# Kernel tuning notes

Hardware: AMD Instinct MI355X
Metric: run time of the kernel (lower is better)

## Reference

```python
import jax, jax.numpy as jnp
import numpy as np

N, E, D, H = 50000, 800000, 128, 8
HD = D // H
EPS = 1e-5


def _layernorm(x, w, b):
    # Custom LayerNorm from the repo: divides by (unbiased std + eps), not sqrt(var+eps)
    mu = x.mean(axis=-1, keepdims=True)
    sd = x.std(axis=-1, keepdims=True, ddof=1)
    return (x - mu) / (sd + EPS) * w + b


def setup_inputs() -> dict:
    key = jax.random.key(0)
    ks = jax.random.split(key, 16)
    s = 1.0 / np.sqrt(D)
    inp = {
        "feats": jax.random.normal(ks[0], (N, D), jnp.float32),
        "edge_index": jax.random.randint(ks[1], (E, 2), 0, N, jnp.int32),
        "Wq": jax.random.normal(ks[2], (D, D), jnp.float32) * s,
        "bq": jnp.zeros((D,), jnp.float32),
        "Wk": jax.random.normal(ks[3], (D, D), jnp.float32) * s,
        "bk": jnp.zeros((D,), jnp.float32),
        "Wv": jax.random.normal(ks[4], (D, D), jnp.float32) * s,
        "bv": jnp.zeros((D,), jnp.float32),
        "Wo": jax.random.normal(ks[5], (D, D), jnp.float32) * s,
        "bo": jnp.zeros((D,), jnp.float32),
        "ln1_w": jnp.ones((D,), jnp.float32),
        "ln1_b": jnp.zeros((D,), jnp.float32),
        "ln2_w": jnp.ones((D,), jnp.float32),
        "ln2_b": jnp.zeros((D,), jnp.float32),
        "W1": jax.random.normal(ks[6], (4 * D, D), jnp.float32) * s,
        "b1": jnp.zeros((4 * D,), jnp.float32),
        "W2": jax.random.normal(ks[7], (D, 4 * D), jnp.float32) * (1.0 / np.sqrt(4 * D)),
        "b2": jnp.zeros((D,), jnp.float32),
    }
    return inp


def reference(feats, edge_index, Wq, bq, Wk, bk, Wv, bv, Wo, bo,
              ln1_w, ln1_b, ln2_w, ln2_b, W1, b1, W2, b2):
    n = feats.shape[0]
    row, col = edge_index[:, 0], edge_index[:, 1]

    # --- multi-head dot-product attention over edges (dropout = identity, eval mode) ---
    x2 = _layernorm(feats, ln1_w, ln1_b)
    q = (x2 @ Wq.T + bq).reshape(n, H, HD)
    k = (x2 @ Wk.T + bk).reshape(n, H, HD)
    v = (x2 @ Wv.T + bv).reshape(n, H, HD)

    # per-edge scores: q[col] . k[row] / sqrt(head_dim)  -> [E, H]
    scores = jnp.einsum('ehd,ehd->eh', q[col], k[row]) / np.sqrt(HD).astype(np.float32)

    # scatter softmax normalized over groups of `row`
    smax = jax.ops.segment_max(scores, row, num_segments=n)       # [N, H]
    ex = jnp.exp(scores - smax[row])                              # [E, H]
    denom = jax.ops.segment_sum(ex, row, num_segments=n)         # [N, H]
    alpha = ex / denom[row]                                       # [E, H]

    # weighted messages, aggregated at col via scatter_add
    msg = alpha[:, :, None] * v[row]                              # [E, H, HD]
    agg = jax.ops.segment_sum(msg, col, num_segments=n).reshape(n, D)
    att = agg @ Wo.T + bo

    feats = feats + att  # residual 1

    # --- MLP block: note ReLU after BOTH linears (fc_dims=[4D, D], D != 1) ---
    x2 = _layernorm(feats, ln2_w, ln2_b)
    h = jax.nn.relu(x2 @ W1.T + b1)
    h = jax.nn.relu(h @ W2.T + b2)
    feats = feats + h  # residual 2
    return feats
```

## Files before the change

kernel.cpp:

```cpp
#include <hip/hip_runtime.h>
#include <hip/hip_bf16.h>
#include <math.h>

#define H_HEADS 8
constexpr float LN_EPS = 1e-5f;
constexpr int NBCH = 64;
constexpr int NSEG = 4;

using short8 = __attribute__((ext_vector_type(8))) short;
using f32x4  = __attribute__((ext_vector_type(4))) float;
using half2v = __attribute__((ext_vector_type(2))) _Float16;

#if defined(__has_builtin)
#  if __has_builtin(__builtin_amdgcn_fdot2)
#    define HAS_FDOT2 1
#  endif
#endif
#ifndef HAS_FDOT2
#  define HAS_FDOT2 0
#endif

__device__ __forceinline__ ushort f2bf(float v){
  __hip_bfloat16 h = __float2bfloat16(v);
  return *reinterpret_cast<ushort*>(&h);
}
__device__ __forceinline__ float bf2f(ushort u){
  return __uint_as_float(((unsigned)u) << 16);
}

__device__ __forceinline__ void stage16(const ushort* g, ushort* l){
  __builtin_amdgcn_global_load_lds((const __attribute__((address_space(1))) unsigned*)g,
                                   (__attribute__((address_space(3))) unsigned*)l,
                                   16, 0, 0);
}

__global__ void ln_kernel(const float* __restrict__ x, const float* __restrict__ w,
                          const float* __restrict__ b, ushort* __restrict__ out, int nrows){
  int wid = threadIdx.x >> 6, lane = threadIdx.x & 63;
  int r = blockIdx.x * (blockDim.x >> 6) + wid;
  if (r >= nrows) return;
  float2 v = ((const float2*)(x + (size_t)r*128))[lane];
  float s = v.x + v.y;
  #pragma unroll
  for (int o = 32; o; o >>= 1) s += __shfl_xor(s, o);
  float mu = s * (1.0f/128.0f);
  float d0 = v.x - mu, d1 = v.y - mu;
  float ss = d0*d0 + d1*d1;
  #pragma unroll
  for (int o = 32; o; o >>= 1) ss += __shfl_xor(ss, o);
  float sd = sqrtf(ss * (1.0f/127.0f));
  float inv = 1.0f / (sd + LN_EPS);
  float2 wv = ((const float2*)w)[lane];
  float2 bv = ((const float2*)b)[lane];
  ushort2 o2 = { f2bf(d0*inv*wv.x + bv.x), f2bf(d1*inv*wv.y + bv.y) };
  ((ushort2*)(out + (size_t)r*128))[lane] = o2;
}

struct CvtArgs { const float* s[6]; ushort* d[6]; int cnt[6]; };
__global__ void cvt6_kernel(CvtArgs a){
  int w = blockIdx.y;
  int i = blockIdx.x*blockDim.x + threadIdx.x;
  if (i < a.cnt[w]) a.d[w][i] = f2bf(a.s[w][i]);
}

template<int K, int RELU, int RESID, int OUTMODE>
__device__ __forceinline__ void gemm_lds_body(
    const ushort* __restrict__ A, const ushort* __restrict__ W,
    const float* __restrict__ bias, const float* __restrict__ resid,
    void* __restrict__ out, int M, int Nout, int cb, ushort* Wl){
  constexpr int NCH = K / 128;
  int t = threadIdx.x;
  int wid = t >> 6, lane = t & 63;
  int mb = blockIdx.x * 128 + wid * 16;
  int lrow = lane & 15, kgrp = lane >> 4;
  int row = mb + lrow;
  bool waveok = mb < M;
  bool rowok = row < M;
  const ushort* arow = A + (size_t)(rowok ? row : (M-1)) * K + kgrp*8;

  f32x4 acc[8] = {};
  short8 af[2][4];

  #pragma unroll
  for (int p = 0; p < 4; ++p){
    int L = p*512 + t;
    int colp = L >> 4, sp = L & 15;
    stage16(W + (size_t)colp*K + ((sp ^ (colp & 7)) << 3),
            (ushort*)((char*)Wl + ((size_t)(p*512 + (t & ~63)))*16));
  }
  if (waveok){
    #pragma unroll
    for (int kk = 0; kk < 4; ++kk)
      af[0][kk] = *(const short8*)(arow + kk*32);
  }

  #pragma unroll
  for (int ci = 0; ci < NCH; ++ci){
    __syncthreads();
    int cur = ci & 1;
    if (waveok){
      if (ci + 1 < NCH){
        #pragma unroll
        for (int kk = 0; kk < 4; ++kk)
          af[cur^1][kk] = *(const short8*)(arow + (ci+1)*128 + kk*32);
      }
      #pragma unroll
      for (int kk = 0; kk < 4; ++kk){
        #pragma unroll
        for (int nt = 0; nt < 8; ++nt){
          int colc = nt*16 + lrow;
          int g = kk*4 + kgrp;
          short8 bfv = *(const short8*)((const char*)Wl + colc*256 + ((g ^ (colc & 7))*16));
          acc[nt] = __builtin_amdgcn_mfma_f32_16x16x32_bf16(af[cur][kk], bfv, acc[nt], 0, 0, 0);
        }
      }
    }
    if (ci + 1 < NCH){
      __syncthreads();
      const ushort* Wc = W + (ci+1)*128;
      #pragma unroll
      for (int p = 0; p < 4; ++p){
        int L = p*512 + t;
        int colp = L >> 4, sp = L & 15;
        stage16(Wc + (size_t)colp*K + ((sp ^ (colp & 7)) << 3),
                (ushort*)((char*)Wl + ((size_t)(p*512 + (t & ~63)))*16));
      }
    }
  }
  if (!waveok) return;

  int r0 = mb + kgrp*4;
  #pragma unroll
  for (int nt = 0; nt < 8; ++nt){
    int c = cb + nt*16 + lrow;
    float bsum = bias[c];
    #pragma unroll
    for (int i = 0; i < 4; ++i){
      int r = r0 + i;
      if (r >= M) continue;
      float v = acc[nt][i] + bsum;
      if (RELU)  v = fmaxf(v, 0.0f);
      if (RESID) v += resid[(size_t)r*Nout + c];
      if (OUTMODE == 1) ((ushort*)out)[(size_t)r*Nout + c] = f2bf(v);
      else if (OUTMODE == 2){
        _Float16 hv = (_Float16)v;
        ((ushort*)out)[(size_t)r*Nout + c] = __builtin_bit_cast(ushort, hv);
      } else ((float*)out)[(size_t)r*Nout + c] = v;
    }
  }
}

template<int K, int RELU, int RESID, int OUTMODE>
__global__ __launch_bounds__(512) void gemm_lds(
    const ushort* __restrict__ A, const ushort* __restrict__ Wfull,
    const float* __restrict__ bias, const float* __restrict__ resid,
    void* __restrict__ out, int M, int Nout){
  __shared__ __align__(16) ushort Wl[16384];
  int cb = blockIdx.y * 128;
  gemm_lds_body<K,RELU,RESID,OUTMODE>(A, Wfull + (size_t)cb*K, bias, resid, out, M, Nout, cb, Wl);
}

__global__ __launch_bounds__(512) void qkv_lds(
    const ushort* __restrict__ A, const ushort* __restrict__ Wcat,
    const float* __restrict__ bq, const float* __restrict__ bk, const float* __restrict__ bv,
    ushort* __restrict__ qb, ushort* __restrict__ kb, ushort* __restrict__ vb, int M){
  __shared__ __align__(16) ushort Wl[16384];
  int y = blockIdx.y;
  const float* bias = (y==0) ? bq : (y==1) ? bk : bv;
  ushort* out = (y==0) ? qb : (y==1) ? kb : vb;
  if (y == 2)
    gemm_lds_body<128,0,0,1>(A, Wcat + (size_t)y*16384, bias, nullptr, out, M, 128, 0, Wl);
  else
    gemm_lds_body<128,0,0,2>(A, Wcat + (size_t)y*16384, bias, nullptr, out, M, 128, 0, Wl);
}

__global__ __launch_bounds__(512) void gemm_wo_ln2(
    const ushort* __restrict__ A, const ushort* __restrict__ W,
    const float* __restrict__ bias, const float* __restrict__ feats,
    const float* __restrict__ lnw, const float* __restrict__ lnb,
    float* __restrict__ outp, ushort* __restrict__ x2b, int M){
  constexpr int K = 128;
  __shared__ __align__(16) ushort Wl[16384];
  int t = threadIdx.x;
  int wid = t >> 6, lane = t & 63;
  int mb = blockIdx.x * 128 + wid * 16;
  int lrow = lane & 15, kgrp = lane >> 4;
  int row = mb + lrow;
  bool waveok = mb < M;
  bool rowok = row < M;
  const ushort* arow = A + (size_t)(rowok ? row : (M-1)) * K + kgrp*8;

  f32x4 acc[8] = {};
  short8 af[4];

  #pragma unroll
  for (int p = 0; p < 4; ++p){
    int L = p*512 + t;
    int colp = L >> 4, sp = L & 15;
    stage16(W + (size_t)colp*K + ((sp ^ (colp & 7)) << 3),
            (ushort*)((char*)Wl + ((size_t)(p*512 + (t & ~63)))*16));
  }
  if (waveok){
    #pragma unroll
    for (int kk = 0; kk < 4; ++kk)
      af[kk] = *(const short8*)(arow + kk*32);
  }
  __syncthreads();
  if (!waveok) return;

  #pragma unroll
  for (int kk = 0; kk < 4; ++kk){
    #pragma unroll
    for (int nt = 0; nt < 8; ++nt){
      int colc = nt*16 + lrow;
      int g = kk*4 + kgrp;
      short8 bfv = *(const short8*)((const char*)Wl + colc*256 + ((g ^ (colc & 7))*16));
      acc[nt] = __builtin_amdgcn_mfma_f32_16x16x32_bf16(af[kk], bfv, acc[nt], 0, 0, 0);
    }
  }

  int r0 = mb + kgrp*4;
  float vv[8][4];
  float lw[8], lb[8];
  #pragma unroll
  for (int nt = 0; nt < 8; ++nt){
    int c = nt*16 + lrow;
    float bsum = bias[c];
    lw[nt] = lnw[c]; lb[nt] = lnb[c];
    #pragma unroll
    for (int i = 0; i < 4; ++i){
      int r = r0 + i;
      float v = 0.f;
      if (r < M){
        v = acc[nt][i] + bsum + feats[(size_t)r*128 + c];
        outp[(size_t)r*128 + c] = v;
      }
      vv[nt][i] = v;
    }
  }
  #pragma unroll
  for (int i = 0; i < 4; ++i){
    int r = r0 + i;
    float s = 0.f;
    #pragma unroll
    for (int nt = 0; nt < 8; ++nt) s += vv[nt][i];
    #pragma unroll
    for (int o = 1; o < 16; o <<= 1) s += __shfl_xor(s, o);
    float mu = s * (1.0f/128.0f);
    float ss = 0.f;
    float d[8];
    #pragma unroll
    for (int nt = 0; nt < 8; ++nt){ d[nt] = vv[nt][i] - mu; ss += d[nt]*d[nt]; }
    #pragma unroll
    for (int o = 1; o < 16; o <<= 1) ss += __shfl_xor(ss, o);
    float sd = sqrtf(ss * (1.0f/127.0f));
    float inv = 1.0f / (sd + LN_EPS);
    if (r < M){
      #pragma unroll
      for (int nt = 0; nt < 8; ++nt){
        int c = nt*16 + lrow;
        x2b[(size_t)r*128 + c] = f2bf(d[nt]*inv*lw[nt] + lb[nt]);
      }
    }
  }
}

__global__ __launch_bounds__(256) void hist_seg2(const int* __restrict__ ei,
    unsigned* __restrict__ copies, int E, int n, int nw, int chunk, int nsb){
  __shared__ unsigned hh[12544];
  int b = blockIdx.x, s = blockIdx.y, t = threadIdx.x;
  int bin0 = s * nsb;
  int bin1 = min(bin0 + nsb, n);
  int words = (bin1 - bin0 + 1) >> 1;
  for (int i = t; i < 2*words; i += 256) hh[i] = 0;
  __syncthreads();
  int lo = b*chunk, hi = min(lo + chunk, E);
  for (int e = lo + t; e < hi; e += 256){
    int2 rc = ((const int2*)ei)[e];
    if (rc.x >= bin0 && rc.x < bin1)
      atomicAdd(&hh[(rc.x - bin0) >> 1], 1u << ((rc.x & 1)*16));
    if (rc.y >= bin0 && rc.y < bin1)
      atomicAdd(&hh[words + ((rc.y - bin0) >> 1)], 1u << ((rc.y & 1)*16));
  }
  __syncthreads();
  unsigned* d0 = copies + (size_t)b*nw + (bin0 >> 1);
  unsigned* d1 = copies + (size_t)(NBCH + b)*nw + (bin0 >> 1);
  for (int i = t; i < words; i += 256){ d0[i] = hh[i]; d1[i] = hh[words + i]; }
}

__global__ __launch_bounds__(256) void scan_fold(const unsigned* __restrict__ copies,
    int* __restrict__ cnt2, ushort* __restrict__ choff, int n, int nw){
  int y = blockIdx.y;
  int bin = blockIdx.x*256 + threadIdx.x;
  if (bin >= n) return;
  const unsigned* cp = copies + (size_t)y*NBCH*nw + (bin >> 1);
  int sh = (bin & 1)*16;
  int run = 0;
  for (int b = 0; b < NBCH; ++b){
    int c = (int)((cp[(size_t)b*nw] >> sh) & 0xffffu);
    choff[((size_t)y*NBCH + b)*n + bin] = (ushort)run;
    run += c;
  }
  cnt2[(size_t)y*n + bin] = run;
}

__global__ __launch_bounds__(256) void scan_reduce(const int* __restrict__ cnt0,
                                                   int* __restrict__ partial, int n, int nb){
  const int* cnt = cnt0 + (size_t)blockIdx.y * n;
  int t = threadIdx.x;
  int base = blockIdx.x*1024 + t*4;
  int s = 0;
  #pragma unroll
  for (int j = 0; j < 4; ++j){ int i = base+j; if (i < n) s += cnt[i]; }
  __shared__ int sm[256];
  sm[t] = s; __syncthreads();
  for (int off = 128; off; off >>= 1){
    if (t < off) sm[t] += sm[t+off];
    __syncthreads();
  }
  if (t == 0) partial[blockIdx.y*nb + blockIdx.x] = sm[0];
}

__global__ __launch_bounds__(256) void scan_mid(int* __restrict__ partial, int nb,
                                                int* __restrict__ rptr, int* __restrict__ cptr, int n){
  int y = blockIdx.y;
  int* p = partial + y*nb;
  int t = threadIdx.x;
  __shared__ int sm[256];
  sm[t] = (t < nb) ? p[t] : 0;
  __syncthreads();
  for (int off = 1; off < 256; off <<= 1){
    int v = (t >= off) ? sm[t-off] : 0;
    __syncthreads();
    sm[t] += v;
    __syncthreads();
  }
  if (t < nb) p[t] = (t == 0) ? 0 : sm[t-1];
  if (t == 0) (y ? cptr : rptr)[n] = sm[255];
}

__global__ __launch_bounds__(256) void scan_scatter(const int* __restrict__ cnt0,
                                                    const int* __restrict__ partial,
                                                    int* __restrict__ rptr, int* __restrict__ cptr,
                                                    int n, int nb){
  int y = blockIdx.y;
  const int* cnt = cnt0 + (size_t)y * n;
  int* ptr = y ? cptr : rptr;
  int t = threadIdx.x;
  int base = blockIdx.x*1024 + t*4;
  int v[4]; int s = 0;
  #pragma unroll
  for (int j = 0; j < 4; ++j){ int i = base+j; v[j] = (i<n)?cnt[i]:0; s += v[j]; }
  __shared__ int sm[256];
  sm[t] = s; __syncthreads();
  for (int off = 1; off < 256; off <<= 1){
    int x = (t >= off) ? sm[t-off] : 0;
    __syncthreads();
    sm[t] += x;
    __syncthreads();
  }
  int pre = partial[y*nb + blockIdx.x] + ((t==0)?0:sm[t-1]);
  #pragma unroll
  for (int j = 0; j < 4; ++j){
    int i = base+j;
    if (i < n){ ptr[i] = pre; pre += v[j]; }
  }
}

__global__ __launch_bounds__(256) void fill_r_seg(const int* __restrict__ ei,
    const int* __restrict__ rptr, const ushort* __restrict__ choffR,
    int* __restrict__ rcol, int* __restrict__ pose, int E, int n, int chunk, int nsb){
  __shared__ unsigned hh[8192];
  int b = blockIdx.x, s = blockIdx.y, t = threadIdx.x;
  int bin0 = s * nsb;
  int bin1 = min(bin0 + nsb, n);
  int words = (bin1 - bin0 + 1) >> 1;
  for (int i = t; i < words; i += 256) hh[i] = 0;
  __syncthreads();
  const ushort* chb = choffR + (size_t)b*n;
  int lo = b*chunk, hi = min(lo + chunk, E);
  for (int e = lo + t; e < hi; e += 256){
    int2 rc = ((const int2*)ei)[e];
    int bin = rc.x;
    if (bin < bin0 || bin >= bin1) continue;
    int sh = (bin & 1)*16;
    unsigned old = atomicAdd(&hh[(bin - bin0) >> 1], 1u << sh);
    int rank = (int)((old >> sh) & 0xffffu);
    int pos = rptr[bin] + (int)chb[bin] + rank;
    rcol[pos] = rc.y;
    pose[e] = pos;
  }
}

__global__ __launch_bounds__(256) void fill_c_seg(const int* __restrict__ ei,
    const int* __restrict__ cptr, const ushort* __restrict__ choffC,
    const int* __restrict__ pose, int* __restrict__ crow, int* __restrict__ cposr,
    int E, int n, int chunk, int nsb){
  __shared__ unsigned hh[8192];
  int b = blockIdx.x, s = blockIdx.y, t = threadIdx.x;
  int bin0 = s * nsb;
  int bin1 = min(bin0 + nsb, n);
  int words = (bin1 - bin0 + 1) >> 1;
  for (int i = t; i < words; i += 256) hh[i] = 0;
  __syncthreads();
  const ushort* chb = choffC + (size_t)b*n;
  int lo = b*chunk, hi = min(lo + chunk, E);
  for (int e = lo + t; e < hi; e += 256){
    int2 rc = ((const int2*)ei)[e];
    int bin = rc.y;
    if (bin < bin0 || bin >= bin1) continue;
    int sh = (bin & 1)*16;
    unsigned old = atomicAdd(&hh[(bin - bin0) >> 1], 1u << sh);
    int rank = (int)((old >> sh) & 0xffffu);
    int pos = cptr[bin] + (int)chb[bin] + rank;
    crow[pos] = rc.x;
    cposr[pose[e]] = pos;
  }
}

__device__ __forceinline__ float qdot16h(const ushort* __restrict__ qb, int c, int h,
                                         const half2v* kf2){
  const int4* qp = (const int4*)(qb + (size_t)c*128 + h*16);
  int4 a = qp[0], b = qp[1];
  int qa[8] = {a.x, a.y, a.z, a.w, b.x, b.y, b.z, b.w};
  float s = 0.f;
#if HAS_FDOT2
  #pragma unroll
  for (int i = 0; i < 8; ++i)
    s = __builtin_amdgcn_fdot2(__builtin_bit_cast(half2v, qa[i]), kf2[i], s, false);
#else
  #pragma unroll
  for (int i = 0; i < 8; ++i){
    half2v q2 = __builtin_bit_cast(half2v, qa[i]);
    s += (float)q2.x * (float)kf2[i].x + (float)q2.y * (float)kf2[i].y;
  }
#endif
  return s * 0.25f;
}

template<int NS>
__device__ __forceinline__ void softmax_rows(const ushort* __restrict__ qb,
    const int* __restrict__ rcol, const int* __restrict__ cposr,
    ushort* __restrict__ cbuf, const half2v* kf2, int lo, int hi, int h, int el,
    int rl, int cpl){
  float sreg[NS];
  float m = -1e30f;
  #pragma unroll
  for (int ts = 0; ts < NS; ++ts){
    int c = __shfl(rl, el + ts*8);
    int j = lo + el + ts*8;
    float s = -1e30f;
    if (j < hi) s = qdot16h(qb, c, h, kf2);
    sreg[ts] = s;
    m = fmaxf(m, s);
  }
  if (NS == 8)
    for (int j = lo + el + 64; j < hi; j += 8)
      m = fmaxf(m, qdot16h(qb, rcol[j], h, kf2));
  #pragma unroll
  for (int o = 8; o < 64; o <<= 1) m = fmaxf(m, __shfl_xor(m, o));

  float d = 0.f;
  #pragma unroll
  for (int ts = 0; ts < NS; ++ts){
    int j = lo + el + ts*8;
    if (j < hi){ float e = __expf(sreg[ts] - m); sreg[ts] = e; d += e; }
  }
  if (NS == 8)
    for (int j = lo + el + 64; j < hi; j += 8)
      d += __expf(qdot16h(qb, rcol[j], h, kf2) - m);
  #pragma unroll
  for (int o = 8; o < 64; o <<= 1) d += __shfl_xor(d, o);
  float invd = 1.0f / d;

  #pragma unroll
  for (int ts = 0; ts < NS; ++ts){
    int cp = __shfl(cpl, el + ts*8);
    int j = lo + el + ts*8;
    if (j < hi) cbuf[(size_t)cp*8 + h] = f2bf(sreg[ts] * invd);
  }
  if (NS == 8)
    for (int j = lo + el + 64; j < hi; j += 8){
      float s = qdot16h(qb, rcol[j], h, kf2);
      cbuf[(size_t)cposr[j]*8 + h] = f2bf(__expf(s - m) * invd);
    }
}

__global__ void row_softmax_kernel(const ushort* __restrict__ qb, const ushort* __restrict__ kb,
                                   const int* __restrict__ rptr, const int* __restrict__ rcol,
                                   const int* __restrict__ cposr,
                                   ushort* __restrict__ cbuf, int n){
  int wid = threadIdx.x >> 6, lane = threadIdx.x & 63;
  int r = blockIdx.x * (blockDim.x >> 6) + wid;
  if (r >= n) return;
  int lo = rptr[r], hi = rptr[r+1];
  if (lo >= hi) return;
  int h = lane & 7, el = lane >> 3;

  int jl = lo + lane;
  bool jok = jl < hi;
  int rl  = rcol [jok ? jl : lo];
  int cpl = cposr[jok ? jl : lo];

  half2v kf2[8];
  {
    const int4* kp = (const int4*)(kb + (size_t)r*128 + h*16);
    int4 k0 = kp[0], k1 = kp[1];
    kf2[0] = __builtin_bit_cast(half2v, k0.x);
    kf2[1] = __builtin_bit_cast(half2v, k0.y);
    kf2[2] = __builtin_bit_cast(half2v, k0.z);
    kf2[3] = __builtin_bit_cast(half2v, k0.w);
    kf2[4] = __builtin_bit_cast(half2v, k1.x);
    kf2[5] = __builtin_bit_cast(half2v, k1.y);
    kf2[6] = __builtin_bit_cast(half2v, k1.z);
    kf2[7] = __builtin_bit_cast(half2v, k1.w);
  }

  int deg = hi - lo;
  if (deg <= 16)      softmax_rows<2>(qb, rcol, cposr, cbuf, kf2, lo, hi, h, el, rl, cpl);
  else if (deg <= 32) softmax_rows<4>(qb, rcol, cposr, cbuf, kf2, lo, hi, h, el, rl, cpl);
  else                softmax_rows<8>(qb, rcol, cposr, cbuf, kf2, lo, hi, h, el, rl, cpl);
}

__global__ void agg_kernel(const ushort* __restrict__ vb, const ushort* __restrict__ cbuf,
                           const int* __restrict__ cptr, const int* __restrict__ crow,
                           ushort* __restrict__ aggb, int n){
  int wid = threadIdx.x >> 6, lane = threadIdx.x & 63;
  int node = blockIdx.x * (blockDim.x >> 6) + wid;
  if (node >= n) return;
  int lo = cptr[node], hi = cptr[node+1];
  int deg = hi - lo;
  int oct = lane >> 3, l8 = lane & 7;

  int jl = lo + lane;
  int crl = crow[jl < hi ? jl : lo];

  float acc[16] = {};
  int tmax = (deg + 7) >> 3;
  for (int ts = 0; ts < tmax; ++ts){
    int li = oct + ts*8;
    int row = __shfl(crl, li & 63);
    if (li < deg){
      if (li >= 64) row = crow[lo + li];
      float a = bf2f(cbuf[(size_t)(lo + li)*8 + l8]);
      const short8* vp = (const short8*)(vb + (size_t)row*128 + l8*16);
      short8 v0 = vp[0], v1 = vp[1];
      #pragma unroll
      for (int i = 0; i < 8; ++i){
        acc[i]   = fmaf(a, bf2f((ushort)v0[i]), acc[i]);
        acc[8+i] = fmaf(a, bf2f((ushort)v1[i]), acc[8+i]);
      }
    }
  }
  #pragma unroll
  for (int i = 0; i < 16; ++i){
    acc[i] += __shfl_xor(acc[i], 8);
    acc[i] += __shfl_xor(acc[i], 16);
    acc[i] += __shfl_xor(acc[i], 32);
  }
  if (oct == 0){
    short8 o0, o1;
    #pragma unroll
    for (int i = 0; i < 8; ++i){ o0[i] = (short)f2bf(acc[i]); o1[i] = (short)f2bf(acc[8+i]); }
    short8* op = (short8*)(aggb + (size_t)node*128 + l8*16);
    op[0] = o0; op[1] = o1;
  }
}

extern "C" void kernel_launch(void* const* d_in, const int* in_sizes, int n_in,
                              void* d_out, int out_size, void* d_ws, size_t ws_size,
                              hipStream_t stream){
  const float* feats = (const float*)d_in[0];
  const int*   ei    = (const int*)  d_in[1];
  const float* Wq = (const float*)d_in[2];
  const float* bq = (const float*)d_in[3];
  const float* Wk = (const float*)d_in[4];
  const float* bk = (const float*)d_in[5];
  const float* Wv = (const float*)d_in[6];
  const float* bv = (const float*)d_in[7];
  const float* Wo = (const float*)d_in[8];
  const float* bo = (const float*)d_in[9];
  const float* ln1w = (const float*)d_in[10];
  const float* ln1b = (const float*)d_in[11];
  const float* ln2w = (const float*)d_in[12];
  const float* ln2b = (const float*)d_in[13];
  const float* W1 = (const float*)d_in[14];
  const float* b1 = (const float*)d_in[15];
  const float* W2 = (const float*)d_in[16];
  const float* b2 = (const float*)d_in[17];
  float* outp = (float*)d_out;

  int n = in_sizes[0] / 128;
  int E = in_sizes[1] / 2;
  int nw = (n + 1) >> 1;
  int chunk = (E + NBCH - 1) / NBCH;
  int nsb = (((n + NSEG - 1) / NSEG) + 1) & ~1;

  const size_t ND  = (size_t)n * 128;
  const size_t ND2 = ND / 2;
  const size_t EH  = (size_t)E * H_HEADS;

  float* ws = (float*)d_ws;
  ushort* x2b  = (ushort*)ws;
  ushort* qb   = (ushort*)(ws + ND2);
  ushort* kb   = (ushort*)(ws + 2*ND2);
  ushort* vb   = (ushort*)(ws + 3*ND2);
  ushort* cbuf = (ushort*)(ws + 4*ND2);
  ushort* aggb = (ushort*)(ws + 4*ND2 + EH/2);
  int* crow    = (int*)(ws + 5*ND2 + EH/2);
  int* cposr   = crow + E;
  int* rcol    = cposr + E;
  int* pose    = rcol + E;
  int* rptr    = pose + E;
  int* cptr    = rptr + (n + 4);
  int* cnt2    = cptr + (n + 4);
  ushort* choff = (ushort*)(cnt2 + 2*n);
  unsigned* copies = (unsigned*)(choff + (size_t)2*NBCH*n);
  int* partial = (int*)(copies + (size_t)2*NBCH*nw);
  ushort* wbuf = (ushort*)(partial + 512);
  ushort* Wqb = wbuf;
  ushort* Wkb = Wqb + 16384;
  ushort* Wvb = Wkb + 16384;
  ushort* Wob = Wvb + 16384;
  ushort* W1b = Wob + 16384;
  ushort* W2b = W1b + 65536;
  ushort* h1  = qb;

  CvtArgs ca;
  ca.s[0]=Wq; ca.s[1]=Wk; ca.s[2]=Wv; ca.s[3]=Wo; ca.s[4]=W1; ca.s[5]=W2;
  ca.d[0]=Wqb; ca.d[1]=Wkb; ca.d[2]=Wvb; ca.d[3]=Wob; ca.d[4]=W1b; ca.d[5]=W2b;
  ca.cnt[0]=ca.cnt[1]=ca.cnt[2]=ca.cnt[3]=16384; ca.cnt[4]=ca.cnt[5]=65536;
  cvt6_kernel<<<dim3(65536/256, 6), 256, 0, stream>>>(ca);

  int nb = (n + 1023)/1024;
  hist_seg2 <<<dim3(NBCH,NSEG), 256, 0, stream>>>(ei, copies, E, n, nw, chunk, nsb);
  scan_fold <<<dim3((n+255)/256,2), 256, 0, stream>>>(copies, cnt2, choff, n, nw);
  scan_reduce <<<dim3(nb,2), 256, 0, stream>>>(cnt2, partial, n, nb);
  scan_mid    <<<dim3(1,2),  256, 0, stream>>>(partial, nb, rptr, cptr, n);
  scan_scatter<<<dim3(nb,2), 256, 0, stream>>>(cnt2, partial, rptr, cptr, n, nb);
  fill_r_seg<<<dim3(NBCH,NSEG), 256, 0, stream>>>(ei, rptr, choff,                  rcol, pose, E, n, chunk, nsb);
  fill_c_seg<<<dim3(NBCH,NSEG), 256, 0, stream>>>(ei, cptr, choff + (size_t)NBCH*n, pose, crow, cposr, E, n, chunk, nsb);

  ln_kernel<<<(n+3)/4, 256, 0, stream>>>(feats, ln1w, ln1b, x2b, n);

  int gm = (n + 127)/128;
  qkv_lds<<<dim3(gm,3), 512, 0, stream>>>(x2b, Wqb, bq, bk, bv, qb, kb, vb, n);

  row_softmax_kernel<<<(n+3)/4, 256, 0, stream>>>(qb, kb, rptr, rcol, cposr, cbuf, n);

  agg_kernel<<<(n+3)/4, 256, 0, stream>>>(vb, cbuf, cptr, crow, aggb, n);

  gemm_wo_ln2<<<gm, 512, 0, stream>>>(aggb, Wob, bo, feats, ln2w, ln2b, outp, x2b, n);

  gemm_lds<128,1,0,1><<<dim3(gm,4), 512, 0, stream>>>(x2b, W1b, b1, nullptr, h1,  n, 512);
  gemm_lds<512,1,1,0><<<dim3(gm,1), 512, 0, stream>>>(h1,  W2b, b2, outp,    outp, n, 128);
}
```

Measured before the change: 282.7 us.

## Store Q in FP8 and fuse QKV projections into one kernel

Q is now written as FP8 (e4m3-style) instead of fp16, which halves the bytes gathered per edge in the row softmax kernel. The Q dot product decodes FP8 to float and accumulates with fma, and K is pre-expanded to float registers. The three QKV projections now share one block, loading the A tile once and looping over the three weight matrices in LDS, rather than running as three grid-y blocks. The cost is lower precision on attention scores, extra decode ALU work and register pressure, and fewer blocks in the QKV launch.

```diff
diff --git a/kernel.cpp b/kernel.cpp
--- a/kernel.cpp
+++ b/kernel.cpp
@@ -9,16 +9,23 @@
 
 using short8 = __attribute__((ext_vector_type(8))) short;
 using f32x4  = __attribute__((ext_vector_type(4))) float;
+using f32x2  = __attribute__((ext_vector_type(2))) float;
 using half2v = __attribute__((ext_vector_type(2))) _Float16;
 
 #if defined(__has_builtin)
 #  if __has_builtin(__builtin_amdgcn_fdot2)
 #    define HAS_FDOT2 1
+#  endif
+#  if __has_builtin(__builtin_amdgcn_cvt_pk_f32_fp8) && __has_builtin(__builtin_amdgcn_cvt_pk_fp8_f32)
+#    define HAS_CVT_FP8 1
 #  endif
 #endif
 #ifndef HAS_FDOT2
 #  define HAS_FDOT2 0
 #endif
+#ifndef HAS_CVT_FP8
+#  define HAS_CVT_FP8 0
+#endif
 
 __device__ __forceinline__ ushort f2bf(float v){
   __hip_bfloat16 h = __float2bfloat16(v);
@@ -26,6 +33,27 @@
 }
 __device__ __forceinline__ float bf2f(ushort u){
   return __uint_as_float(((unsigned)u) << 16);
+}
+
+__device__ __forceinline__ unsigned char f32_to_fp8(float v){
+#if HAS_CVT_FP8
+  return (unsigned char)(__builtin_amdgcn_cvt_pk_fp8_f32(v, v, 0, false) & 0xff);
+#else
+  _Float16 hv = (_Float16)v;
+  ushort h = __builtin_bit_cast(ushort, hv);
+  unsigned sign = (h >> 8) & 0x80;
+  unsigned p = h & 0x7fff;
+  if (p < 0x2400u) return (unsigned char)sign;
+  unsigned q = (p - 0x2000u + 0x40u) >> 7;
+  if (q > 0x7eu) q = 0x7eu;
+  return (unsigned char)(sign | q);
+#endif
+}
+__device__ __forceinline__ float fp8_to_f32(unsigned b){
+  unsigned p = b & 0x7f;
+  ushort hbits = (ushort)(((b & 0x80) << 8) | (p ? ((p << 7) + 0x2000u) : 0));
+  _Float16 hv = __builtin_bit_cast(_Float16, hbits);
+  return (float)hv;
 }
 
 __device__ __forceinline__ void stage16(const ushort* g, ushort* l){
@@ -160,18 +188,72 @@
   gemm_lds_body<K,RELU,RESID,OUTMODE>(A, Wfull + (size_t)cb*K, bias, resid, out, M, Nout, cb, Wl);
 }
 
-__global__ __launch_bounds__(512) void qkv_lds(
+__global__ __launch_bounds__(512) void qkv_fused(
     const ushort* __restrict__ A, const ushort* __restrict__ Wcat,
     const float* __restrict__ bq, const float* __restrict__ bk, const float* __restrict__ bv,
-    ushort* __restrict__ qb, ushort* __restrict__ kb, ushort* __restrict__ vb, int M){
+    unsigned char* __restrict__ qb8, ushort* __restrict__ kb, ushort* __restrict__ vb, int M){
+  constexpr int K = 128;
   __shared__ __align__(16) ushort Wl[16384];
-  int y = blockIdx.y;
-  const float* bias = (y==0) ? bq : (y==1) ? bk : bv;
-  ushort* out = (y==0) ? qb : (y==1) ? kb : vb;
-  if (y == 2)
-    gemm_lds_body<128,0,0,1>(A, Wcat + (size_t)y*16384, bias, nullptr, out, M, 128, 0, Wl);
-  else
-    gemm_lds_body<128,0,0,2>(A, Wcat + (size_t)y*16384, bias, nullptr, out, M, 128, 0, Wl);
+  int t = threadIdx.x;
+  int wid = t >> 6, lane = t & 63;
+  int mb = blockIdx.x * 128 + wid * 16;
+  int lrow = lane & 15, kgrp = lane >> 4;
+  int row = mb + lrow;
+  bool waveok = mb < M;
+  bool rowok = row < M;
+  const ushort* arow = A + (size_t)(rowok ? row : (M-1)) * K + kgrp*8;
+
+  short8 af[4];
+  if (waveok){
+    #pragma unroll
+    for (int kk = 0; kk < 4; ++kk)
+      af[kk] = *(const short8*)(arow + kk*32);
+  }
+
+  #pragma unroll
+  for (int y = 0; y < 3; ++y){
+    if (y) __syncthreads();
+    const ushort* W = Wcat + (size_t)y*16384;
+    #pragma unroll
+    for (int p = 0; p < 4; ++p){
+      int L = p*512 + t;
+      int colp = L >> 4, sp = L & 15;
+      stage16(W + (size_t)colp*K + ((sp ^ (colp & 7)) << 3),
+              (ushort*)((char*)Wl + ((size_t)(p*512 + (t & ~63)))*16));
+    }
+    __syncthreads();
+    if (waveok){
+      const float* bias = (y==0) ? bq : (y==1) ? bk : bv;
+      f32x4 acc[8] = {};
+      #pragma unroll
+      for (int kk = 0; kk < 4; ++kk){
+        #pragma unroll
+        for (int nt = 0; nt < 8; ++nt){
+          int colc = nt*16 + lrow;
+          int g = kk*4 + kgrp;
+          short8 bfv = *(const short8*)((const char*)Wl + colc*256 + ((g ^ (colc & 7))*16));
+          acc[nt] = __builtin_amdgcn_mfma_f32_16x16x32_bf16(af[kk], bfv, acc[nt], 0, 0, 0);
+        }
+      }
+      int r0 = mb + kgrp*4;
+      #pragma unroll
+      for (int nt = 0; nt < 8; ++nt){
+        int c = nt*16 + lrow;
+        float bsum = bias[c];
+        #pragma unroll
+        for (int i = 0; i < 4; ++i){
+          int r = r0 + i;
+          if (r >= M) continue;
+          float v = acc[nt][i] + bsum;
+          if (y == 0)      qb8[(size_t)r*128 + c] = f32_to_fp8(v);
+          else if (y == 1){
+            _Float16 hv = (_Float16)v;
+            kb[(size_t)r*128 + c] = __builtin_bit_cast(ushort, hv);
+          } else           vb[(size_t)r*128 + c] = f2bf(v);
+        }
+      }
+    }
+  }
 }
 
 __global__ __launch_bounds__(512) void gemm_wo_ln2(
@@ -418,30 +500,34 @@
   }
 }
 
-__device__ __forceinline__ float qdot16h(const ushort* __restrict__ qb, int c, int h,
-                                         const half2v* kf2){
-  const int4* qp = (const int4*)(qb + (size_t)c*128 + h*16);
-  int4 a = qp[0], b = qp[1];
-  int qa[8] = {a.x, a.y, a.z, a.w, b.x, b.y, b.z, b.w};
+__device__ __forceinline__ float qdot16q8(const unsigned char* __restrict__ qb8, int c, int h,
+                                          const float* kf){
+  const uint4* qp = (const uint4*)(qb8 + (size_t)c*128 + h*16);
+  uint4 q = *qp;
+  unsigned w[4] = {q.x, q.y, q.z, q.w};
   float s = 0.f;
-#if HAS_FDOT2
-  #pragma unroll
-  for (int i = 0; i < 8; ++i)
-    s = __builtin_amdgcn_fdot2(__builtin_bit_cast(half2v, qa[i]), kf2[i], s, false);
+  #pragma unroll
+  for (int i = 0; i < 4; ++i){
+#if HAS_CVT_FP8
+    f32x2 lo = __builtin_amdgcn_cvt_pk_f32_fp8(w[i], false);
+    f32x2 hi = __builtin_amdgcn_cvt_pk_f32_fp8(w[i], true);
+    s = fmaf(lo[0], kf[4*i+0], s);
+    s = fmaf(lo[1], kf[4*i+1], s);
+    s = fmaf(hi[0], kf[4*i+2], s);
+    s = fmaf(hi[1], kf[4*i+3], s);
 #else
-  #pragma unroll
-  for (int i = 0; i < 8; ++i){
-    half2v q2 = __builtin_bit_cast(half2v, qa[i]);
-    s += (float)q2.x * (float)kf2[i].x + (float)q2.y * (float)kf2[i].y;
-  }
+    #pragma unroll
+    for (int j = 0; j < 4; ++j)
+      s = fmaf(fp8_to_f32((w[i] >> (8*j)) & 0xffu), kf[4*i+j], s);
 #endif
+  }
   return s * 0.25f;
 }
 
 template<int NS>
-__device__ __forceinline__ void softmax_rows(const ushort* __restrict__ qb,
+__device__ __forceinline__ void softmax_rows(const unsigned char* __restrict__ qb8,
     const int* __restrict__ rcol, const int* __restrict__ cposr,
-    ushort* __restrict__ cbuf, const half2v* kf2, int lo, int hi, int h, int el,
+    ushort* __restrict__ cbuf, const float* kf, int lo, int hi, int h, int el,
     int rl, int cpl){
   float sreg[NS];
   float m = -1e30f;
@@ -450,13 +536,13 @@
     int c = __shfl(rl, el + ts*8);
     int j = lo + el + ts*8;
     float s = -1e30f;
-    if (j < hi) s = qdot16h(qb, c, h, kf2);
+    if (j < hi) s = qdot16q8(qb8, c, h, kf);
     sreg[ts] = s;
     m = fmaxf(m, s);
   }
   if (NS == 8)
     for (int j = lo + el + 64; j < hi; j += 8)
-      m = fmaxf(m, qdot16h(qb, rcol[j], h, kf2));
+      m = fmaxf(m, qdot16q8(qb8, rcol[j], h, kf));
   #pragma unroll
   for (int o = 8; o < 64; o <<= 1) m = fmaxf(m, __shfl_xor(m, o));
 
@@ -468,7 +554,7 @@
   }
   if (NS == 8)
     for (int j = lo + el + 64; j < hi; j += 8)
-      d += __expf(qdot16h(qb, rcol[j], h, kf2) - m);
+      d += __expf(qdot16q8(qb8, rcol[j], h, kf) - m);
   #pragma unroll
   for (int o = 8; o < 64; o <<= 1) d += __shfl_xor(d, o);
   float invd = 1.0f / d;
@@ -481,12 +567,13 @@
   }
   if (NS == 8)
     for (int j = lo + el + 64; j < hi; j += 8){
-      float s = qdot16h(qb, rcol[j], h, kf2);
+      float s = qdot16q8(qb8, rcol[j], h, kf);
       cbuf[(size_t)cposr[j]*8 + h] = f2bf(__expf(s - m) * invd);
     }
 }
 
-__global__ void row_softmax_kernel(const ushort* __restrict__ qb, const ushort* __restrict__ kb,
+__global__ void row_softmax_kernel(const unsigned char* __restrict__ qb8,
+                                   const ushort* __restrict__ kb,
                                    const int* __restrict__ rptr, const int* __restrict__ rcol,
                                    const int* __restrict__ cposr,
                                    ushort* __restrict__ cbuf, int n){
@@ -502,24 +589,23 @@
   int rl  = rcol [jok ? jl : lo];
   int cpl = cposr[jok ? jl : lo];
 
-  half2v kf2[8];
+  float kf[16];
   {
     const int4* kp = (const int4*)(kb + (size_t)r*128 + h*16);
     int4 k0 = kp[0], k1 = kp[1];
-    kf2[0] = __builtin_bit_cast(half2v, k0.x);
-    kf2[1] = __builtin_bit_cast(half2v, k0.y);
-    kf2[2] = __builtin_bit_cast(half2v, k0.z);
-    kf2[3] = __builtin_bit_cast(half2v, k0.w);
-    kf2[4] = __builtin_bit_cast(half2v, k1.x);
-    kf2[5] = __builtin_bit_cast(half2v, k1.y);
-    kf2[6] = __builtin_bit_cast(half2v, k1.z);
-    kf2[7] = __builtin_bit_cast(half2v, k1.w);
+    int kw[8] = {k0.x,k0.y,k0.z,k0.w,k1.x,k1.y,k1.z,k1.w};
+    #pragma unroll
+    for (int i = 0; i < 8; ++i){
+      half2v k2 = __builtin_bit_cast(half2v, kw[i]);
+      kf[2*i]   = (float)k2.x;
+      kf[2*i+1] = (float)k2.y;
+    }
   }
 
   int deg = hi - lo;
-  if (deg <= 16)      softmax_rows<2>(qb, rcol, cposr, cbuf, kf2, lo, hi, h, el, rl, cpl);
-  else if (deg <= 32) softmax_rows<4>(qb, rcol, cposr, cbuf, kf2, lo, hi, h, el, rl, cpl);
-  else                softmax_rows<8>(qb, rcol, cposr, cbuf, kf2, lo, hi, h, el, rl, cpl);
+  if (deg <= 16)      softmax_rows<2>(qb8, rcol, cposr, cbuf, kf, lo, hi, h, el, rl, cpl);
+  else if (deg <= 32) softmax_rows<4>(qb8, rcol, cposr, cbuf, kf, lo, hi, h, el, rl, cpl);
+  else                softmax_rows<8>(qb8, rcol, cposr, cbuf, kf, lo, hi, h, el, rl, cpl);
 }
 
 __global__ void agg_kernel(const ushort* __restrict__ vb, const ushort* __restrict__ cbuf,
@@ -602,7 +688,7 @@
 
   float* ws = (float*)d_ws;
   ushort* x2b  = (ushort*)ws;
-  ushort* qb   = (ushort*)(ws + ND2);
+  unsigned char* qb8 = (unsigned char*)(ws + ND2);
   ushort* kb   = (ushort*)(ws + 2*ND2);
   ushort* vb   = (ushort*)(ws + 3*ND2);
   ushort* cbuf = (ushort*)(ws + 4*ND2);
@@ -624,7 +710,7 @@
   ushort* Wob = Wvb + 16384;
   ushort* W1b = Wob + 16384;
   ushort* W2b = W1b + 65536;
-  ushort* h1  = qb;
+  ushort* h1  = (ushort*)qb8;
 
   CvtArgs ca;
   ca.s[0]=Wq; ca.s[1]=Wk; ca.s[2]=Wv; ca.s[3]=Wo; ca.s[4]=W1; ca.s[5]=W2;
@@ -644,9 +730,9 @@
   ln_kernel<<<(n+3)/4, 256, 0, stream>>>(feats, ln1w, ln1b, x2b, n);
 
   int gm = (n + 127)/128;
-  qkv_lds<<<dim3(gm,3), 512, 0, stream>>>(x2b, Wqb, bq, bk, bv, qb, kb, vb, n);
-
-  row_softmax_kernel<<<(n+3)/4, 256, 0, stream>>>(qb, kb, rptr, rcol, cposr, cbuf, n);
+  qkv_fused<<<gm, 512, 0, stream>>>(x2b, Wqb, bq, bk, bv, qb8, kb, vb, n);
+
+  row_softmax_kernel<<<(n+3)/4, 256, 0, stream>>>(qb8, kb, rptr, rcol, cposr, cbuf, n);
 
   agg_kernel<<<(n+3)/4, 256, 0, stream>>>(vb, cbuf, cptr, crow, aggb, n);
 
```

Result: faster. 274.6 us (-2.8%).
